# Performance work log

Hardware: AMD Instinct MI355X
Metric: run time of the kernel (lower is better)

## Reference

```python
import jax, jax.numpy as jnp
import numpy as np

NC = 5        # num_class
NS = 2        # n_sigma
MAX_ID = 3    # candidate instance ids per class: 1..MAX_ID
W_INST, W_VAR, W_SEED = 1.0, 10.0, 1.0
GRID = 1024   # size of the registered xym buffer
H = W = 768
CLASS_WEIGHT = np.ones((NC,), np.float32)


def _xym(h, w):
    # buffer built at GRID resolution, then sliced [0:h, 0:w] (matches torch)
    base = jnp.linspace(0.0, 1.0, GRID)
    xm = jnp.broadcast_to(base[None, :w], (h, w))  # x varies along width
    ym = jnp.broadcast_to(base[:h, None], (h, w))  # y varies along height
    return jnp.stack([xm, ym], 0)  # [2,h,w]


def _lovasz_flat(logits, labels_f):
    # standard flat Lovasz hinge
    signs = 2.0 * labels_f - 1.0
    errors = 1.0 - logits * signs
    perm = jnp.argsort(-errors)  # descending errors
    errors_sorted = errors[perm]
    gt_sorted = labels_f[perm]
    gts = jnp.sum(gt_sorted)
    inter = gts - jnp.cumsum(gt_sorted)
    union = gts + jnp.cumsum(1.0 - gt_sorted)
    jac = 1.0 - inter / union
    jac = jnp.concatenate([jac[:1], jac[1:] - jac[:-1]])
    return jnp.dot(jax.nn.relu(errors_sorted), jax.lax.stop_gradient(jac))


def _per_image(pred, inst, lab, xyf, cw):
    h, w = lab.shape
    n = h * w
    embf = jnp.tanh(pred[0:2]).reshape(2, n) + xyf          # spatial embedding [2,N]
    sigf = pred[2:2 + NS].reshape(NS, n)                     # sigma [NS,N]
    seedf = jax.nn.sigmoid(pred[2 + NS:2 + NS + NC]).reshape(NC, n)  # seed maps [NC,N]
    labf = lab.reshape(n)
    instf = inst.reshape(n)

    cls = jnp.arange(1, NC + 1)
    # background seed loss per class: sum(seed^2) over pixels where label != cl
    bg = labf[None, :] != cls[:, None]
    seed_bg = jnp.sum(jnp.where(bg, seedf, 0.0) ** 2)

    cl_pair = jnp.repeat(cls, MAX_ID)                       # [P]
    id_pair = jnp.tile(jnp.arange(1, MAX_ID + 1), NC)       # [P]

    def per_inst(cl, iid):
        ci = cl - 1
        m = (labf == cl) & (instf == iid)                   # [N]
        mf = m.astype(embf.dtype)
        cnt = jnp.sum(mf)
        valid = cnt > 0
        cnts = jnp.maximum(cnt, 1.0)
        # approximate medoid: per-dim lower median of masked coords,
        # then masked pixel closest to the median
        xy_sorted = jnp.sort(jnp.where(m[None, :], xyf, 2.0), axis=1)
        mid = jnp.maximum((cnt.astype(jnp.int32) - 1) // 2, 0)
        med = jnp.take(xy_sorted, mid, axis=1)              # [2]
        d = jnp.sum((xyf - med[:, None]) ** 2, axis=0)
        imin = jnp.argmin(jnp.where(m, d, jnp.inf))
        center = jnp.take(xyf, imin, axis=1)                # [2], constant wrt params
        s_mean = jnp.sum(sigf * mf[None, :], axis=1) / cnts  # [NS]
        var = jnp.sum(mf[None, :] * (sigf - jax.lax.stop_gradient(s_mean)[:, None]) ** 2) / (cnts * NS)
        s = jnp.exp(s_mean * 10.0)                           # [NS]
        dist = jnp.exp(-jnp.sum((embf - center[:, None]) ** 2 * s[:, None], axis=0))  # [N]
        lov = _lovasz_flat(dist * 2.0 - 1.0, mf)
        seedc = jnp.take(seedf, ci, axis=0)
        seed_in = jnp.sum(mf * (seedc - jax.lax.stop_gradient(dist)) ** 2)
        return valid, var, lov, seed_in

    valid, var, lov, seed_in = jax.vmap(per_inst)(cl_pair, id_pair)
    vf = valid.astype(embf.dtype)
    objs = jnp.maximum(jnp.sum(vf), 1.0)
    w_pair = jnp.take(cw, cl_pair - 1)
    seed_loss = (seed_bg + jnp.sum(w_pair * seed_in * vf)) / n
    return (W_INST * jnp.sum(lov * vf) / objs
            + W_VAR * jnp.sum(var * vf) / objs
            + W_SEED * seed_loss)


def setup_inputs() -> dict:
    key = jax.random.key(0)
    k1, k2, k3 = jax.random.split(key, 3)
    prediction = jax.random.normal(k1, (2, 2 + NS + NC, H, W), dtype=jnp.float32)
    instances = jax.random.randint(k2, (2, H, W), 0, MAX_ID + 1, dtype=jnp.int32)
    labels = jax.random.randint(k3, (2, H, W), 0, NC + 1, dtype=jnp.int32)
    return {"prediction": prediction, "instances": instances, "labels": labels}


def reference(prediction, instances, labels):
    xyf = _xym(H, W).reshape(2, H * W)
    cw = jnp.asarray(CLASS_WEIGHT)
    losses = jax.vmap(lambda p, i, l: _per_image(p, i, l, xyf, cw))(prediction, instances, labels)
    return jnp.mean(losses)
```

## Files before the change

kernel.cpp:

```cpp
#include <hip/hip_runtime.h>
#include <cstddef>
#include <cstdint>


#define HH 768
#define WW 768
#define NPIX (HH*WW)
#define NCL 5
#define MAXID 3
#define PAIRS (NCL*MAXID)
#define NIMG 2
#define NCH 9
#define BINS 256
#define HPXB 2304
#define HNB (NPIX/HPXB)
#define TX 12
#define TY 32
#define XW 64
#define YH 24
#define BPI (TX*TY)

struct P1 {
  unsigned short col[PAIRS][XW];
  unsigned short row[PAIRS][YH];
  float sig0[PAIRS], sig1[PAIRS];
  float sT, sO;
};

struct WS {
  unsigned long long argkey[NIMG][PAIRS];
  unsigned int cnt[NIMG][PAIRS];
  unsigned int lovdone;
  unsigned int pad0;
  alignas(8) unsigned int hall[NIMG][PAIRS][2][BINS];
  float varsum[NIMG][PAIRS];
  float seedin[NIMG][PAIRS];
  float medx[NIMG][PAIRS], medy[NIMG][PAIRS];
  float s0a[NIMG][PAIRS], s1a[NIMG][PAIRS];
  float sm0a[NIMG][PAIRS], sm1a[NIMG][PAIRS];
  float validf[NIMG][PAIRS], cntf[NIMG][PAIRS];
  float lov[NIMG][PAIRS];
  float seedT[NIMG], seedOwn[NIMG];
  alignas(16) float2 emb[NIMG][NPIX];
  unsigned char pridx[NIMG][NPIX];
  alignas(4) P1 part[NIMG][BPI];
};

__device__ __forceinline__ float basef(int i) {
  return (float)i * (1.0f / 1023.0f);
}
__device__ __forceinline__ int pair_of(int l, int it) {
  return (l >= 1 && l <= NCL && it >= 1 && it <= MAXID) ? (l - 1) * MAXID + (it - 1) : -1;
}
__device__ __forceinline__ float fast_sigmoid(float z) {
  return __fdividef(1.f, 1.f + __expf(-z));
}
__device__ __forceinline__ float fast_tanh(float x) {
  float xc = fminf(fmaxf(x, -15.f), 15.f);
  float e = __expf(2.f * xc);
  return __fdividef(e - 1.f, e + 1.f);
}

__global__ __launch_bounds__(256) void k_pass1(const float* __restrict__ pred,
                                               const int* __restrict__ inst,
                                               const int* __restrict__ lab,
                                               WS* __restrict__ ws) {
  int img = blockIdx.z;
  int x0 = blockIdx.x * XW;
  int y0 = blockIdx.y * YH;
  int tid = threadIdx.x, lane = tid & 63, wv = tid >> 6;
  const float* p = pred + (size_t)img * NCH * NPIX;
  const int* lb = lab + (size_t)img * NPIX;
  const int* ib = inst + (size_t)img * NPIX;

  __shared__ unsigned int lcol[PAIRS][XW];
  __shared__ unsigned int lrow[PAIRS][YH];
  __shared__ float lsig0[PAIRS], lsig1[PAIRS];
  __shared__ float fred0[4], fred1[4];
  for (int k = tid; k < PAIRS * XW; k += 256) ((unsigned int*)lcol)[k] = 0;
  for (int k = tid; k < PAIRS * YH; k += 256) ((unsigned int*)lrow)[k] = 0;
  if (tid < PAIRS) { lsig0[tid] = 0.f; lsig1[tid] = 0.f; }
  __syncthreads();

  int x = x0 + lane;
  float bx = basef(x);
  float t = 0.f, own = 0.f;
#pragma unroll
  for (int i = 0; i < YH / 4; i++) {
    int y = y0 + wv + 4 * i;
    int pix = y * WW + x;
    int l = lb[pix];
    int it = ib[pix];
    float s, q;
    s = fast_sigmoid(p[4 * NPIX + pix]); q = s * s; t += q; if (l == 1) own += q;
    s = fast_sigmoid(p[5 * NPIX + pix]); q = s * s; t += q; if (l == 2) own += q;
    s = fast_sigmoid(p[6 * NPIX + pix]); q = s * s; t += q; if (l == 3) own += q;
    s = fast_sigmoid(p[7 * NPIX + pix]); q = s * s; t += q; if (l == 4) own += q;
    s = fast_sigmoid(p[8 * NPIX + pix]); q = s * s; t += q; if (l == 5) own += q;
    float e0 = fast_tanh(p[0 * NPIX + pix]) + bx;
    float e1 = fast_tanh(p[1 * NPIX + pix]) + basef(y);
    ws->emb[img][pix] = make_float2(e0, e1);
    int pr = pair_of(l, it);
    ws->pridx[img][pix] = (unsigned char)(pr >= 0 ? pr : 255);
    if (pr >= 0) {
      atomicAdd(&lcol[pr][lane], 1u);
      atomicAdd(&lrow[pr][y - y0], 1u);
      atomicAdd(&lsig0[pr], p[2 * NPIX + pix]);
      atomicAdd(&lsig1[pr], p[3 * NPIX + pix]);
    }
  }
  for (int o = 32; o; o >>= 1) { t += __shfl_down(t, o); own += __shfl_down(own, o); }
  if (lane == 0) { fred0[wv] = t; fred1[wv] = own; }
  __syncthreads();

  P1* P = &ws->part[img][blockIdx.x * TY + blockIdx.y];
  const unsigned int* fc = (const unsigned int*)lcol;
  for (int k = tid; k < PAIRS * XW / 2; k += 256) {
    unsigned int lo = fc[2 * k], hi = fc[2 * k + 1];
    ((unsigned int*)P->col)[k] = (lo & 0xFFFFu) | (hi << 16);
  }
  const unsigned int* fr = (const unsigned int*)lrow;
  for (int k = tid; k < PAIRS * YH / 2; k += 256) {
    unsigned int lo = fr[2 * k], hi = fr[2 * k + 1];
    ((unsigned int*)P->row)[k] = (lo & 0xFFFFu) | (hi << 16);
  }
  if (tid < PAIRS) { P->sig0[tid] = lsig0[tid]; P->sig1[tid] = lsig1[tid]; }
  if (tid == 0) {
    P->sT = fred0[0] + fred0[1] + fred0[2] + fred0[3];
    P->sO = fred1[0] + fred1[1] + fred1[2] + fred1[3];
  }
}

__global__ __launch_bounds__(256) void k_medoid(WS* __restrict__ ws) {
  int img = blockIdx.x / PAIRS, p = blockIdx.x % PAIRS;
  const P1* B = ws->part[img];
  int tid = threadIdx.x, lane = tid & 63, wv = tid >> 6;
  __shared__ unsigned int pref[256];
  __shared__ int cross;
  __shared__ float fr0[4], fr1[4];
  unsigned int c = 0;
  int res[2];
#pragma unroll
  for (int h = 0; h < 2; h++) {
    unsigned int v[3];
#pragma unroll
    for (int j = 0; j < 3; j++) {
      int cc = tid * 3 + j;
      unsigned int s = 0;
      if (h == 0) {
        int xt = cc >> 6, ci = cc & 63;
        for (int yt = 0; yt < TY; yt++) s += B[xt * TY + yt].col[p][ci];
      } else {
        int yt = cc / YH, ri = cc % YH;
        for (int xt = 0; xt < TX; xt++) s += B[xt * TY + yt].row[p][ri];
      }
      v[j] = s;
    }
    unsigned int s3 = v[0] + v[1] + v[2];
    pref[tid] = s3;
    __syncthreads();
    for (int d = 1; d < 256; d <<= 1) {
      unsigned int tv = (tid >= d) ? pref[tid - d] : 0u;
      __syncthreads();
      pref[tid] += tv;
      __syncthreads();
    }
    c = pref[255];
    unsigned int target = (c > 0) ? (((c - 1u) >> 1) + 1u) : 1u;
    if (tid == 0) cross = 0;
    __syncthreads();
    unsigned int inc = pref[tid];
    unsigned int exc = inc - s3;
    if (inc >= target && exc < target) {
      int j = (exc + v[0] >= target) ? 0 : ((exc + v[0] + v[1] >= target) ? 1 : 2);
      cross = tid * 3 + j;
    }
    __syncthreads();
    res[h] = cross;
    __syncthreads();
  }
  float s0 = 0.f, s1 = 0.f;
  for (int b = tid; b < BPI; b += 256) { s0 += B[b].sig0[p]; s1 += B[b].sig1[p]; }
  for (int o = 32; o; o >>= 1) { s0 += __shfl_down(s0, o); s1 += __shfl_down(s1, o); }
  if (lane == 0) { fr0[wv] = s0; fr1[wv] = s1; }
  __syncthreads();
  if (tid == 0) {
    float sig0 = fr0[0] + fr0[1] + fr0[2] + fr0[3];
    float sig1 = fr1[0] + fr1[1] + fr1[2] + fr1[3];
    float vf = (c > 0) ? 1.f : 0.f;
    float cf = (c > 0) ? (float)c : 1.f;
    float sm0 = sig0 / cf, sm1 = sig1 / cf;
    ws->cnt[img][p] = c;
    ws->medx[img][p] = basef(res[0]);
    ws->medy[img][p] = basef(res[1]);
    ws->sm0a[img][p] = sm0;
    ws->sm1a[img][p] = sm1;
    ws->s0a[img][p] = __expf(10.f * sm0);
    ws->s1a[img][p] = __expf(10.f * sm1);
    ws->validf[img][p] = vf;
    ws->cntf[img][p] = cf;
  }
  __syncthreads();
  if (p == 0) {
    float a = 0.f, o2 = 0.f;
    for (int b = tid; b < BPI; b += 256) { a += B[b].sT; o2 += B[b].sO; }
    for (int o = 32; o; o >>= 1) { a += __shfl_down(a, o); o2 += __shfl_down(o2, o); }
    if (lane == 0) { fr0[wv] = a; fr1[wv] = o2; }
    __syncthreads();
    if (tid == 0) {
      ws->seedT[img] = fr0[0] + fr0[1] + fr0[2] + fr0[3];
      ws->seedOwn[img] = fr1[0] + fr1[1] + fr1[2] + fr1[3];
    }
  }
}

__global__ __launch_bounds__(256) void k_argmin(WS* __restrict__ ws) {
  int img = blockIdx.y;
  __shared__ unsigned long long skey[PAIRS];
  __shared__ float smx[PAIRS], smy[PAIRS];
  if (threadIdx.x < PAIRS) {
    skey[threadIdx.x] = ~0ULL;
    smx[threadIdx.x] = ws->medx[img][threadIdx.x];
    smy[threadIdx.x] = ws->medy[img][threadIdx.x];
  }
  __syncthreads();
  int px0 = blockIdx.x * 1024 + threadIdx.x * 4;
  uchar4 pr4 = *(const uchar4*)(ws->pridx[img] + px0);
  int y = px0 / WW;
  int x0 = px0 - y * WW;
  float by = basef(y);
#pragma unroll
  for (int k = 0; k < 4; k++) {
    int pr = (k == 0) ? pr4.x : (k == 1) ? pr4.y : (k == 2) ? pr4.z : pr4.w;
    if (pr != 255) {
      int pix = px0 + k;
      float dx = basef(x0 + k) - smx[pr];
      float dy = by - smy[pr];
      float d = dx * dx + dy * dy;
      unsigned long long key = ((unsigned long long)__float_as_uint(d) << 32) | (unsigned int)pix;
      atomicMin(&skey[pr], key);
    }
  }
  __syncthreads();
  if (threadIdx.x < PAIRS && skey[threadIdx.x] != ~0ULL)
    atomicMin(&ws->argkey[img][threadIdx.x], skey[threadIdx.x]);
}

__global__ __launch_bounds__(256) void k_hist(const float* __restrict__ pred,
                                              WS* __restrict__ ws) {
  int img = blockIdx.y;
  int tid = threadIdx.x;
  __shared__ unsigned int h[PAIRS][2][BINS];
  __shared__ float lvar[PAIRS], lseed[PAIRS];
  __shared__ float lm0[PAIRS], lm1[PAIRS];
  unsigned int* hf = &h[0][0][0];
#pragma unroll
  for (int k = 0; k < PAIRS * 2 * BINS / 256; k++) hf[k * 256 + tid] = 0;
  if (tid < PAIRS) {
    lvar[tid] = 0.f; lseed[tid] = 0.f;
    lm0[tid] = ws->sm0a[img][tid]; lm1[tid] = ws->sm1a[img][tid];
  }
  __syncthreads();

  float cxr[PAIRS], cyr[PAIRS], S0r[PAIRS], S1r[PAIRS];
#pragma unroll
  for (int p = 0; p < PAIRS; p++) {
    unsigned long long key = ws->argkey[img][p];
    int imin = (int)(key & 0xffffffffu);
    cxr[p] = basef(imin % WW);
    cyr[p] = basef(imin / WW);
    S0r[p] = ws->s0a[img][p];
    S1r[p] = ws->s1a[img][p];
  }
  const float* pb = pred + (size_t)img * NCH * NPIX;
  const float* embb = (const float*)ws->emb[img];
  const unsigned char* prb = ws->pridx[img];
  int base = blockIdx.x * HPXB;

#pragma unroll 2
  for (int i = 0; i < HPXB / 256; i++) {
    int pix = base + i * 256 + tid;
    float2 e = *(const float2*)(embb + 2 * pix);
    int pp = prb[pix];
    float dOwn = 0.f;
#pragma unroll
    for (int p = 0; p < PAIRS; p++) {
      float dx = e.x - cxr[p];
      float dy = e.y - cyr[p];
      float q = dx * dx * S0r[p] + dy * dy * S1r[p];
      float d = __expf(-q);
      bool m = (pp == p);
      dOwn = m ? d : dOwn;
      float e2 = d + d;
      float err = m ? (2.f - e2) : e2;
      int bin = (int)(err * (BINS * 0.5f));
      bin = bin > (BINS - 1) ? (BINS - 1) : (bin < 0 ? 0 : bin);
      atomicAdd(&h[p][m ? 1 : 0][bin], 1u);
    }
    if (pp != 255) {
      float g0 = pb[2 * NPIX + pix] - lm0[pp];
      float g1 = pb[3 * NPIX + pix] - lm1[pp];
      atomicAdd(&lvar[pp], g0 * g0 + g1 * g1);
      float sd = fast_sigmoid(pb[(4 + pp / MAXID) * NPIX + pix]) - dOwn;
      atomicAdd(&lseed[pp], sd * sd);
    }
  }
  __syncthreads();
  unsigned long long* gh = (unsigned long long*)&ws->hall[img][0][0][0];
#pragma unroll
  for (int k = tid * 2; k < PAIRS * 2 * BINS; k += 512) {
    unsigned long long v = (unsigned long long)hf[k] |
                           ((unsigned long long)hf[k + 1] << 32);
    if (v) atomicAdd(&gh[k >> 1], v);
  }
  if (tid < PAIRS) {
    if (lvar[tid] != 0.f) atomicAdd(&ws->varsum[img][tid], lvar[tid]);
    if (lseed[tid] != 0.f) atomicAdd(&ws->seedin[img][tid], lseed[tid]);
  }
}

__global__ __launch_bounds__(256) void k_lovasz(WS* __restrict__ ws, float* __restrict__ out) {
  int b = blockIdx.x / PAIRS, p = blockIdx.x % PAIRS;
  unsigned int gts = ws->cnt[b][p];
  int tid = threadIdx.x;
  float lv = 0.f;
  __shared__ unsigned int sin_s[BINS], sout_s[BINS];
  if (gts != 0) {
    sin_s[tid] = ws->hall[b][p][1][tid];
    sout_s[tid] = ws->hall[b][p][0][tid];
    __syncthreads();
    for (int d = 1; d < BINS; d <<= 1) {
      unsigned int a = (tid + d < BINS) ? sin_s[tid + d] : 0u;
      unsigned int c = (tid + d < BINS) ? sout_s[tid + d] : 0u;
      __syncthreads();
      sin_s[tid] += a; sout_s[tid] += c;
      __syncthreads();
    }
    float gtsf = (float)gts;
    float js = 0.f;
    if (tid >= 1) {
      unsigned int Sin = sin_s[tid], Sout = sout_s[tid];
      js = 1.f - (float)(gts - Sin) / (gtsf + (float)Sout);
    }
    for (int o = 32; o; o >>= 1) js += __shfl_down(js, o);
    __shared__ float wsum[4];
    if ((tid & 63) == 0) wsum[tid >> 6] = js;
    __syncthreads();
    if (tid == 0)
      lv = (2.f / BINS) * (0.5f + wsum[0] + wsum[1] + wsum[2] + wsum[3]);
  }
  __shared__ int amLast;
  if (tid == 0) {
    atomicExch(&ws->lov[b][p], lv);
    __threadfence();
    unsigned int old = atomicAdd(&ws->lovdone, 1u);
    amLast = (old == NIMG * PAIRS - 1);
  }
  __syncthreads();
  if (amLast) {
    __shared__ float rl[NIMG], rv[NIMG], rs[NIMG], ro[NIMG];
    if (tid < NIMG) { rl[tid] = 0.f; rv[tid] = 0.f; rs[tid] = 0.f; ro[tid] = 0.f; }
    __syncthreads();
    if (tid < NIMG * PAIRS) {
      int bb = tid / PAIRS, pp = tid % PAIRS;
      float vf = ws->validf[bb][pp];
      float lvv = atomicAdd(&ws->lov[bb][pp], 0.f);
      atomicAdd(&rl[bb], vf * lvv);
      atomicAdd(&rv[bb], vf * ws->varsum[bb][pp] / (ws->cntf[bb][pp] * 2.f));
      atomicAdd(&rs[bb], vf * ws->seedin[bb][pp]);
      atomicAdd(&ro[bb], vf);
    }
    __syncthreads();
    if (tid == 0) {
      float tot = 0.f;
      for (int bb = 0; bb < NIMG; bb++) {
        float objs = ro[bb] < 1.f ? 1.f : ro[bb];
        float seed_bg = ws->seedT[bb] - ws->seedOwn[bb];
        float seed_loss = (seed_bg + rs[bb]) / (float)NPIX;
        tot += rl[bb] / objs + 10.f * rv[bb] / objs + seed_loss;
      }
      out[0] = tot * 0.5f;
    }
  }
}

extern "C" void kernel_launch(void* const* d_in, const int* in_sizes, int n_in,
                              void* d_out, int out_size, void* d_ws, size_t ws_size,
                              hipStream_t stream) {
  const float* pred = (const float*)d_in[0];
  const int* inst = (const int*)d_in[1];
  const int* lab = (const int*)d_in[2];
  WS* ws = (WS*)d_ws;

  size_t zoff = offsetof(WS, cnt);
  size_t zend = offsetof(WS, medx);
  hipMemsetAsync((char*)d_ws, 0xFF, zoff, stream);
  hipMemsetAsync((char*)d_ws + zoff, 0, zend - zoff, stream);

  k_pass1<<<dim3(TX, TY, NIMG), 256, 0, stream>>>(pred, inst, lab, ws);
  k_medoid<<<dim3(NIMG * PAIRS), 256, 0, stream>>>(ws);
  k_argmin<<<dim3(NPIX / 1024, NIMG), 256, 0, stream>>>(ws);
  k_hist<<<dim3(HNB, NIMG), 256, 0, stream>>>(pred, ws);
  k_lovasz<<<dim3(NIMG * PAIRS), 256, 0, stream>>>(ws, (float*)d_out);
}
```

Baseline: 95.82 us.

## Fold workspace init into pass1, transpose partials, pack histogram bins to 16-bit

Removes the two memset launches by zeroing the accumulator region and setting argmin keys inside k_pass1. Partial column/row counts are stored transposed so k_medoid reads contiguous packed shorts instead of strided struct fields. k_argmin uses fewer blocks, each looping over more pixels, to cut global atomics. k_hist moves to 512 threads with histograms packed as two 16-bit counters per word, halving shared memory, and uses simpler bin arithmetic. Risks: 16-bit shared counters could overflow if one block puts more than 65535 hits in a single bin, and in-kernel zeroing relies on k_pass1 running before any kernel reads those accumulators.

```diff
diff --git a/kernel.cpp b/kernel.cpp
--- a/kernel.cpp
+++ b/kernel.cpp
@@ -12,38 +12,38 @@
 #define NIMG 2
 #define NCH 9
 #define BINS 256
-#define HPXB 2304
+#define HPXB 2048
 #define HNB (NPIX/HPXB)
 #define TX 12
 #define TY 32
 #define XW 64
 #define YH 24
 #define BPI (TX*TY)
-
-struct P1 {
-  unsigned short col[PAIRS][XW];
-  unsigned short row[PAIRS][YH];
-  float sig0[PAIRS], sig1[PAIRS];
-  float sT, sO;
-};
+#define ANB 64
+#define APXB (NPIX/ANB)
 
 struct WS {
-  unsigned long long argkey[NIMG][PAIRS];
-  unsigned int cnt[NIMG][PAIRS];
-  unsigned int lovdone;
-  unsigned int pad0;
   alignas(8) unsigned int hall[NIMG][PAIRS][2][BINS];
   float varsum[NIMG][PAIRS];
   float seedin[NIMG][PAIRS];
+  unsigned int lovdone;
+  unsigned int zpad[3];
+  unsigned long long argkey[NIMG][PAIRS];
   float medx[NIMG][PAIRS], medy[NIMG][PAIRS];
   float s0a[NIMG][PAIRS], s1a[NIMG][PAIRS];
   float sm0a[NIMG][PAIRS], sm1a[NIMG][PAIRS];
   float validf[NIMG][PAIRS], cntf[NIMG][PAIRS];
   float lov[NIMG][PAIRS];
   float seedT[NIMG], seedOwn[NIMG];
+  unsigned int cnt[NIMG][PAIRS];
   alignas(16) float2 emb[NIMG][NPIX];
   unsigned char pridx[NIMG][NPIX];
-  alignas(4) P1 part[NIMG][BPI];
+  alignas(64) unsigned short colpart[NIMG][PAIRS][WW][TY];
+  alignas(64) unsigned short rowpart[NIMG][PAIRS][HH][TX];
+  float sig0part[NIMG][PAIRS][BPI];
+  float sig1part[NIMG][PAIRS][BPI];
+  float sTpart[NIMG][BPI];
+  float sOpart[NIMG][BPI];
 };
 
 __device__ __forceinline__ float basef(int i) {
@@ -66,9 +66,20 @@
                                                const int* __restrict__ lab,
                                                WS* __restrict__ ws) {
   int img = blockIdx.z;
-  int x0 = blockIdx.x * XW;
-  int y0 = blockIdx.y * YH;
+  int xt = blockIdx.x, yt = blockIdx.y;
+  int x0 = xt * XW;
+  int y0 = yt * YH;
   int tid = threadIdx.x, lane = tid & 63, wv = tid >> 6;
+
+  {
+    const int ZN = (int)(offsetof(WS, argkey) / 4);
+    int bid = (blockIdx.z * TY + blockIdx.y) * TX + blockIdx.x;
+    int idx = bid * 256 + tid;
+    if (idx < ZN) ((unsigned int*)ws)[idx] = 0u;
+    if (bid == 0 && tid < NIMG * PAIRS)
+      ((unsigned long long*)ws->argkey)[tid] = ~0ULL;
+  }
+
   const float* p = pred + (size_t)img * NCH * NPIX;
   const int* lb = lab + (size_t)img * NPIX;
   const int* ib = inst + (size_t)img * NPIX;
@@ -113,27 +124,27 @@
   if (lane == 0) { fred0[wv] = t; fred1[wv] = own; }
   __syncthreads();
 
-  P1* P = &ws->part[img][blockIdx.x * TY + blockIdx.y];
-  const unsigned int* fc = (const unsigned int*)lcol;
-  for (int k = tid; k < PAIRS * XW / 2; k += 256) {
-    unsigned int lo = fc[2 * k], hi = fc[2 * k + 1];
-    ((unsigned int*)P->col)[k] = (lo & 0xFFFFu) | (hi << 16);
-  }
-  const unsigned int* fr = (const unsigned int*)lrow;
-  for (int k = tid; k < PAIRS * YH / 2; k += 256) {
-    unsigned int lo = fr[2 * k], hi = fr[2 * k + 1];
-    ((unsigned int*)P->row)[k] = (lo & 0xFFFFu) | (hi << 16);
-  }
-  if (tid < PAIRS) { P->sig0[tid] = lsig0[tid]; P->sig1[tid] = lsig1[tid]; }
+  int bi = yt * TX + xt;
+  for (int k = tid; k < PAIRS * XW; k += 256) {
+    int pp = k >> 6, c = k & 63;
+    ws->colpart[img][pp][x0 + c][yt] = (unsigned short)lcol[pp][c];
+  }
+  for (int k = tid; k < PAIRS * YH; k += 256) {
+    int pp = k / YH, r = k % YH;
+    ws->rowpart[img][pp][y0 + r][xt] = (unsigned short)lrow[pp][r];
+  }
+  if (tid < PAIRS) {
+    ws->sig0part[img][tid][bi] = lsig0[tid];
+    ws->sig1part[img][tid][bi] = lsig1[tid];
+  }
   if (tid == 0) {
-    P->sT = fred0[0] + fred0[1] + fred0[2] + fred0[3];
-    P->sO = fred1[0] + fred1[1] + fred1[2] + fred1[3];
+    ws->sTpart[img][bi] = fred0[0] + fred0[1] + fred0[2] + fred0[3];
+    ws->sOpart[img][bi] = fred1[0] + fred1[1] + fred1[2] + fred1[3];
   }
 }
 
 __global__ __launch_bounds__(256) void k_medoid(WS* __restrict__ ws) {
   int img = blockIdx.x / PAIRS, p = blockIdx.x % PAIRS;
-  const P1* B = ws->part[img];
   int tid = threadIdx.x, lane = tid & 63, wv = tid >> 6;
   __shared__ unsigned int pref[256];
   __shared__ int cross;
@@ -148,11 +159,13 @@
       int cc = tid * 3 + j;
       unsigned int s = 0;
       if (h == 0) {
-        int xt = cc >> 6, ci = cc & 63;
-        for (int yt = 0; yt < TY; yt++) s += B[xt * TY + yt].col[p][ci];
+        const unsigned int* w = (const unsigned int*)ws->colpart[img][p][cc];
+#pragma unroll
+        for (int i = 0; i < TY / 2; i++) { unsigned int u = w[i]; s += (u & 0xFFFFu) + (u >> 16); }
       } else {
-        int yt = cc / YH, ri = cc % YH;
-        for (int xt = 0; xt < TX; xt++) s += B[xt * TY + yt].row[p][ri];
+        const unsigned int* w = (const unsigned int*)ws->rowpart[img][p][cc];
+#pragma unroll
+        for (int i = 0; i < TX / 2; i++) { unsigned int u = w[i]; s += (u & 0xFFFFu) + (u >> 16); }
       }
       v[j] = s;
     }
@@ -180,7 +193,7 @@
     __syncthreads();
   }
   float s0 = 0.f, s1 = 0.f;
-  for (int b = tid; b < BPI; b += 256) { s0 += B[b].sig0[p]; s1 += B[b].sig1[p]; }
+  for (int b = tid; b < BPI; b += 256) { s0 += ws->sig0part[img][p][b]; s1 += ws->sig1part[img][p][b]; }
   for (int o = 32; o; o >>= 1) { s0 += __shfl_down(s0, o); s1 += __shfl_down(s1, o); }
   if (lane == 0) { fr0[wv] = s0; fr1[wv] = s1; }
   __syncthreads();
@@ -203,7 +216,7 @@
   __syncthreads();
   if (p == 0) {
     float a = 0.f, o2 = 0.f;
-    for (int b = tid; b < BPI; b += 256) { a += B[b].sT; o2 += B[b].sO; }
+    for (int b = tid; b < BPI; b += 256) { a += ws->sTpart[img][b]; o2 += ws->sOpart[img][b]; }
     for (int o = 32; o; o >>= 1) { a += __shfl_down(a, o); o2 += __shfl_down(o2, o); }
     if (lane == 0) { fr0[wv] = a; fr1[wv] = o2; }
     __syncthreads();
@@ -224,21 +237,25 @@
     smy[threadIdx.x] = ws->medy[img][threadIdx.x];
   }
   __syncthreads();
-  int px0 = blockIdx.x * 1024 + threadIdx.x * 4;
-  uchar4 pr4 = *(const uchar4*)(ws->pridx[img] + px0);
-  int y = px0 / WW;
-  int x0 = px0 - y * WW;
-  float by = basef(y);
-#pragma unroll
-  for (int k = 0; k < 4; k++) {
-    int pr = (k == 0) ? pr4.x : (k == 1) ? pr4.y : (k == 2) ? pr4.z : pr4.w;
-    if (pr != 255) {
-      int pix = px0 + k;
-      float dx = basef(x0 + k) - smx[pr];
-      float dy = by - smy[pr];
-      float d = dx * dx + dy * dy;
-      unsigned long long key = ((unsigned long long)__float_as_uint(d) << 32) | (unsigned int)pix;
-      atomicMin(&skey[pr], key);
+  int base = blockIdx.x * APXB;
+#pragma unroll
+  for (int i = 0; i < APXB / 1024; i++) {
+    int px0 = base + i * 1024 + threadIdx.x * 4;
+    uchar4 pr4 = *(const uchar4*)(ws->pridx[img] + px0);
+    int y = px0 / WW;
+    int x0 = px0 - y * WW;
+    float by = basef(y);
+#pragma unroll
+    for (int k = 0; k < 4; k++) {
+      int pr = (k == 0) ? pr4.x : (k == 1) ? pr4.y : (k == 2) ? pr4.z : pr4.w;
+      if (pr != 255) {
+        int pix = px0 + k;
+        float dx = basef(x0 + k) - smx[pr];
+        float dy = by - smy[pr];
+        float d = dx * dx + dy * dy;
+        unsigned long long key = ((unsigned long long)__float_as_uint(d) << 32) | (unsigned int)pix;
+        atomicMin(&skey[pr], key);
+      }
     }
   }
   __syncthreads();
@@ -246,16 +263,14 @@
     atomicMin(&ws->argkey[img][threadIdx.x], skey[threadIdx.x]);
 }
 
-__global__ __launch_bounds__(256) void k_hist(const float* __restrict__ pred,
+__global__ __launch_bounds__(512) void k_hist(const float* __restrict__ pred,
                                               WS* __restrict__ ws) {
   int img = blockIdx.y;
   int tid = threadIdx.x;
-  __shared__ unsigned int h[PAIRS][2][BINS];
+  __shared__ unsigned int h32[PAIRS * 2 * (BINS / 2)];
   __shared__ float lvar[PAIRS], lseed[PAIRS];
   __shared__ float lm0[PAIRS], lm1[PAIRS];
-  unsigned int* hf = &h[0][0][0];
-#pragma unroll
-  for (int k = 0; k < PAIRS * 2 * BINS / 256; k++) hf[k * 256 + tid] = 0;
+  for (int k = tid; k < PAIRS * 2 * (BINS / 2); k += 512) h32[k] = 0;
   if (tid < PAIRS) {
     lvar[tid] = 0.f; lseed[tid] = 0.f;
     lm0[tid] = ws->sm0a[img][tid]; lm1[tid] = ws->sm1a[img][tid];
@@ -277,9 +292,9 @@
   const unsigned char* prb = ws->pridx[img];
   int base = blockIdx.x * HPXB;
 
-#pragma unroll 2
-  for (int i = 0; i < HPXB / 256; i++) {
-    int pix = base + i * 256 + tid;
+#pragma unroll
+  for (int i = 0; i < HPXB / 512; i++) {
+    int pix = base + i * 512 + tid;
     float2 e = *(const float2*)(embb + 2 * pix);
     int pp = prb[pix];
     float dOwn = 0.f;
@@ -291,11 +306,10 @@
       float d = __expf(-q);
       bool m = (pp == p);
       dOwn = m ? d : dOwn;
-      float e2 = d + d;
-      float err = m ? (2.f - e2) : e2;
-      int bin = (int)(err * (BINS * 0.5f));
-      bin = bin > (BINS - 1) ? (BINS - 1) : (bin < 0 ? 0 : bin);
-      atomicAdd(&h[p][m ? 1 : 0][bin], 1u);
+      int ib = (int)fminf(d * 256.f, 255.f);
+      int bin = m ? (255 - ib) : ib;
+      int hidx = (p * 2 + (m ? 1 : 0)) * BINS + bin;
+      atomicAdd(&h32[hidx >> 1], 1u << ((hidx & 1) * 16));
     }
     if (pp != 255) {
       float g0 = pb[2 * NPIX + pix] - lm0[pp];
@@ -307,11 +321,13 @@
   }
   __syncthreads();
   unsigned long long* gh = (unsigned long long*)&ws->hall[img][0][0][0];
-#pragma unroll
-  for (int k = tid * 2; k < PAIRS * 2 * BINS; k += 512) {
-    unsigned long long v = (unsigned long long)hf[k] |
-                           ((unsigned long long)hf[k + 1] << 32);
-    if (v) atomicAdd(&gh[k >> 1], v);
+  for (int k = tid; k < PAIRS * 2 * (BINS / 2); k += 512) {
+    unsigned int w = h32[k];
+    if (w) {
+      unsigned long long v = (unsigned long long)(w & 0xFFFFu) |
+                             ((unsigned long long)(w >> 16) << 32);
+      atomicAdd(&gh[k], v);
+    }
   }
   if (tid < PAIRS) {
     if (lvar[tid] != 0.f) atomicAdd(&ws->varsum[img][tid], lvar[tid]);
@@ -392,14 +408,9 @@
   const int* lab = (const int*)d_in[2];
   WS* ws = (WS*)d_ws;
 
-  size_t zoff = offsetof(WS, cnt);
-  size_t zend = offsetof(WS, medx);
-  hipMemsetAsync((char*)d_ws, 0xFF, zoff, stream);
-  hipMemsetAsync((char*)d_ws + zoff, 0, zend - zoff, stream);
-
   k_pass1<<<dim3(TX, TY, NIMG), 256, 0, stream>>>(pred, inst, lab, ws);
   k_medoid<<<dim3(NIMG * PAIRS), 256, 0, stream>>>(ws);
-  k_argmin<<<dim3(NPIX / 1024, NIMG), 256, 0, stream>>>(ws);
-  k_hist<<<dim3(HNB, NIMG), 256, 0, stream>>>(pred, ws);
+  k_argmin<<<dim3(ANB, NIMG), 256, 0, stream>>>(ws);
+  k_hist<<<dim3(HNB, NIMG), 512, 0, stream>>>(pred, ws);
   k_lovasz<<<dim3(NIMG * PAIRS), 256, 0, stream>>>(ws, (float*)d_out);
 }
```

Result: faster. 83.19 us (-13.2%).
